# Performance work log

Hardware: AMD Instinct MI355X
Metric: run time of the kernel (lower is better)

The kernel has to match this reference:

```python
import jax, jax.numpy as jnp
import numpy as np

HEAD_NUM = 8
DIM_QK = 64
DIM_V = 64
SPAN = 64
STRIDE = 4


def _sparse_indices(length_q, length_kv):
    # Replicates torch meshgrid index math (static, numpy).
    R = SPAN // STRIDE
    r = np.arange(R)[:, None]              # [R,1]
    c = np.arange(length_q)[None, :]       # [1,Lq]
    # ceil((c-(span-1))/stride) + r, via floor-div identity ceil(a/b) = -((-a)//b)
    qi_col = -((SPAN - 1 - c) // STRIDE) + r   # [R,Lq]
    qi_row = c - STRIDE * qi_col
    valid = (qi_row >= 0) & (qi_row < SPAN) & (qi_col >= 0) & (qi_col < length_kv)
    qc = np.clip(qi_col, 0, length_kv - 1)
    return jnp.asarray(qc, dtype=jnp.int32), jnp.asarray(valid)


def setup_inputs() -> dict:
    key = jax.random.key(0)
    ks = jax.random.split(key, 7)
    B, Lq, Lkv, D = 2, 4096, 1024, 512
    q = jax.random.normal(ks[0], (B, Lq, D), dtype=jnp.float32)
    k = jax.random.normal(ks[1], (B, Lkv, D), dtype=jnp.float32)
    v = jax.random.normal(ks[2], (B, Lkv, D), dtype=jnp.float32)
    Wq = jax.random.normal(ks[3], (D, HEAD_NUM * DIM_QK), dtype=jnp.float32) * 0.05
    Wk = jax.random.normal(ks[4], (D, HEAD_NUM * DIM_QK), dtype=jnp.float32) * 0.05
    Wv = jax.random.normal(ks[5], (D, HEAD_NUM * DIM_V), dtype=jnp.float32) * 0.05
    Wout = jax.random.normal(ks[6], (HEAD_NUM * DIM_V, D), dtype=jnp.float32) * 0.05
    return {"q": q, "k": k, "v": v, "Wq": Wq, "Wk": Wk, "Wv": Wv, "Wout": Wout}


def reference(q, k, v, Wq, Wk, Wv, Wout):
    B, Lq, _ = q.shape
    Lkv = k.shape[1]
    # Projections -> [B, H, L, D]
    Q = (q @ Wq).reshape(B, Lq, HEAD_NUM, DIM_QK).transpose(0, 2, 1, 3)
    K = (k @ Wk).reshape(B, Lkv, HEAD_NUM, DIM_QK).transpose(0, 2, 1, 3)
    V = (v @ Wv).reshape(B, Lkv, HEAD_NUM, DIM_V).transpose(0, 2, 1, 3)
    qc, valid = _sparse_indices(Lq, Lkv)          # [R,Lq]
    Kg = K[:, :, qc, :]                            # [B,H,R,Lq,DQK] gather
    scores = jnp.einsum("bhcd,bhrcd->bhrc", Q, Kg) / jnp.sqrt(jnp.float32(DIM_QK))
    big_neg = jnp.asarray(-1e30, scores.dtype)
    scores = jnp.where(valid[None, None], scores, big_neg)
    w = jax.nn.softmax(scores, axis=2)             # softmax over the R sparse slots
    w = jnp.where(valid[None, None], w, 0.0)
    Vg = V[:, :, qc, :]                            # [B,H,R,Lq,DV] gather
    ctx = jnp.einsum("bhrc,bhrcd->bhcd", w, Vg)   # [B,H,Lq,DV]
    ctx = ctx.transpose(0, 2, 1, 3).reshape(B, Lq, HEAD_NUM * DIM_V)
    return ctx @ Wout
```

## Files before the change

kernel.cpp:

```cpp
#include <hip/hip_runtime.h>
#include <math.h>

#define HN 8
#define DK 64
#define LQ 4096
#define LKV 1024
#define DMODEL 512
#define BATCH 2

typedef unsigned short u16;
typedef unsigned int u32;
typedef __attribute__((ext_vector_type(8))) __bf16 bf16x8;
typedef __attribute__((ext_vector_type(4))) float f32x4;
typedef __attribute__((ext_vector_type(8))) u16 u16x8;

__device__ __forceinline__ u16 f2bf(float f) {
    u32 u = __float_as_uint(f);
    u = u + 0x7fffu + ((u >> 16) & 1u);
    return (u16)(u >> 16);
}
__device__ __forceinline__ float bf2f(u16 u) {
    return __uint_as_float(((u32)u) << 16);
}

__device__ __forceinline__ void gl_lds16(const u16* g, u16* l) {
    __builtin_amdgcn_global_load_lds((const __attribute__((address_space(1))) u32*)g,
                                     (__attribute__((address_space(3))) u32*)l, 16, 0, 0);
}

template <bool BF16OUT>
__device__ __forceinline__ void gemm_body(const u16* __restrict__ A,
                                          const u16* __restrict__ Bt,
                                          void* __restrict__ Cp,
                                          int bx, int by) {
    __shared__ u16 As[128 * 32];
    __shared__ u16 Bs[128 * 32];

    const int tid = threadIdx.x;
    const int lane = tid & 63;
    const int wave = tid >> 6;
    const int wm = (wave >> 1) * 64;
    const int wn = (wave & 1) * 64;
    const int quad = lane >> 4;
    const int l16 = lane & 15;
    const size_t m0 = (size_t)by * 128;
    const size_t n0 = (size_t)bx * 128;

    f32x4 acc[4][4] = {};

    for (int k0 = 0; k0 < 512; k0 += 32) {
#pragma unroll
        for (int i = 0; i < 2; ++i) {
            const int id = i * 256 + tid;
            const int r = id >> 2;
            const int cs = id & 3;
            const int c = cs ^ ((r >> 1) & 3);
            const u16* ga = &A[(m0 + r) * 512 + k0 + c * 8];
            const u16* gb = &Bt[(n0 + r) * 512 + k0 + c * 8];
            u16* la = &As[(size_t)(i * 256 + wave * 64) * 8];
            u16* lb = &Bs[(size_t)(i * 256 + wave * 64) * 8];
            gl_lds16(ga, la);
            gl_lds16(gb, lb);
        }
        __syncthreads();

        bf16x8 af[4], bf[4];
#pragma unroll
        for (int i = 0; i < 4; ++i) {
            const int ra = wm + i * 16 + l16;
            const int ca = quad ^ ((ra >> 1) & 3);
            af[i] = *(const bf16x8*)&As[ra * 32 + ca * 8];
            const int rb = wn + i * 16 + l16;
            const int cb = quad ^ ((rb >> 1) & 3);
            bf[i] = *(const bf16x8*)&Bs[rb * 32 + cb * 8];
        }
#pragma unroll
        for (int i = 0; i < 4; ++i)
#pragma unroll
            for (int j = 0; j < 4; ++j)
                acc[i][j] = __builtin_amdgcn_mfma_f32_16x16x32_bf16(af[i], bf[j], acc[i][j], 0, 0, 0);
        __syncthreads();
    }

#pragma unroll
    for (int i = 0; i < 4; ++i) {
#pragma unroll
        for (int j = 0; j < 4; ++j) {
            const size_t row = m0 + wm + i * 16 + quad * 4;
            const size_t col = n0 + wn + j * 16 + l16;
#pragma unroll
            for (int t = 0; t < 4; ++t) {
                if (BF16OUT)
                    ((u16*)Cp)[(row + t) * 512 + col] = f2bf(acc[i][j][t]);
                else
                    ((float*)Cp)[(row + t) * 512 + col] = acc[i][j][t];
            }
        }
    }
}

__global__ __launch_bounds__(256) void proj_fused(const u16* __restrict__ qb,
                                                  const u16* __restrict__ kb,
                                                  const u16* __restrict__ vb,
                                                  const u16* __restrict__ wqt,
                                                  const u16* __restrict__ wkt,
                                                  const u16* __restrict__ wvt,
                                                  u16* __restrict__ Qb,
                                                  u16* __restrict__ Kb,
                                                  u16* __restrict__ Vb) {
    const int idx = blockIdx.x;
    if (idx < 256)
        gemm_body<true>(qb, wqt, Qb, idx & 3, idx >> 2);
    else if (idx < 320)
        gemm_body<true>(kb, wkt, Kb, (idx - 256) & 3, (idx - 256) >> 2);
    else
        gemm_body<true>(vb, wvt, Vb, (idx - 320) & 3, (idx - 320) >> 2);
}

__global__ __launch_bounds__(256) void gemm_out(const u16* __restrict__ A,
                                                const u16* __restrict__ Bt,
                                                float* __restrict__ C) {
    gemm_body<false>(A, Bt, C, blockIdx.x & 3, blockIdx.x >> 2);
}

__global__ __launch_bounds__(256) void prep(const float* __restrict__ q,
                                            const float* __restrict__ k,
                                            const float* __restrict__ v,
                                            const float* __restrict__ Wq,
                                            const float* __restrict__ Wk,
                                            const float* __restrict__ Wv,
                                            const float* __restrict__ Wout,
                                            u16* __restrict__ qb, u16* __restrict__ kb,
                                            u16* __restrict__ vb,
                                            u16* __restrict__ wqt, u16* __restrict__ wkt,
                                            u16* __restrict__ wvt, u16* __restrict__ wot) {
    __shared__ float tbuf[32][33];
    const int bid = blockIdx.x;
    const int tid = threadIdx.x;

    if (bid < 3072) {
        const float* in;
        u16* outp;
        int i;
        if (bid < 2048)      { in = q; outp = qb; i = bid * 256 + tid; }
        else if (bid < 2560) { in = k; outp = kb; i = (bid - 2048) * 256 + tid; }
        else                 { in = v; outp = vb; i = (bid - 2560) * 256 + tid; }
        const float4 a = ((const float4*)in)[i * 2];
        const float4 b = ((const float4*)in)[i * 2 + 1];
        u16x8 r;
        r[0] = f2bf(a.x); r[1] = f2bf(a.y); r[2] = f2bf(a.z); r[3] = f2bf(a.w);
        r[4] = f2bf(b.x); r[5] = f2bf(b.y); r[6] = f2bf(b.z); r[7] = f2bf(b.w);
        *(u16x8*)&outp[(size_t)i * 8] = r;
    } else {
        const int wb = bid - 3072;
        const int z = wb >> 8;
        const int t = wb & 255;
        const float* W = (z == 0) ? Wq : (z == 1) ? Wk : (z == 2) ? Wv : Wout;
        u16* O = (z == 0) ? wqt : (z == 1) ? wkt : (z == 2) ? wvt : wot;
        const int tx = tid & 31;
        const int ty = tid >> 5;
        const int x = (t & 15) * 32 + tx;
        const int y0 = (t >> 4) * 32;
#pragma unroll
        for (int i = ty; i < 32; i += 8) tbuf[i][tx] = W[(size_t)(y0 + i) * 512 + x];
        __syncthreads();
#pragma unroll
        for (int i = ty; i < 32; i += 8)
            O[(size_t)((t & 15) * 32 + i) * 512 + y0 + tx] = f2bf(tbuf[tx][i]);
    }
}

__global__ __launch_bounds__(256) void attn_f32(const u16* __restrict__ Q,
                                                const u16* __restrict__ K,
                                                const u16* __restrict__ V,
                                                u16* __restrict__ ctx) {
    __shared__ float Ks[80][68];
    __shared__ float Vs[80][68];

    const int tid = threadIdx.x;
    const int c0 = blockIdx.x * 256;
    const int h = blockIdx.y;
    const int b = blockIdx.z;

    const int fd_c0 = (63 - c0) >> 2;
    const int win_lo = (fd_c0 < 0) ? -fd_c0 : 0;

    for (int i = tid; i < 80 * 8; i += 256) {
        int row = i >> 3;
        int d8 = i & 7;
        int col = win_lo + row;
        if (col < LKV) {
            size_t base = ((size_t)(b * LKV + col)) * DMODEL + h * DK + d8 * 8;
            u16x8 k8 = *(const u16x8*)&K[base];
            u16x8 v8 = *(const u16x8*)&V[base];
            float4 ka = make_float4(bf2f(k8[0]), bf2f(k8[1]), bf2f(k8[2]), bf2f(k8[3]));
            float4 kb4 = make_float4(bf2f(k8[4]), bf2f(k8[5]), bf2f(k8[6]), bf2f(k8[7]));
            float4 va = make_float4(bf2f(v8[0]), bf2f(v8[1]), bf2f(v8[2]), bf2f(v8[3]));
            float4 vb4 = make_float4(bf2f(v8[4]), bf2f(v8[5]), bf2f(v8[6]), bf2f(v8[7]));
            *(float4*)&Ks[row][d8 * 8] = ka;
            *(float4*)&Ks[row][d8 * 8 + 4] = kb4;
            *(float4*)&Vs[row][d8 * 8] = va;
            *(float4*)&Vs[row][d8 * 8 + 4] = vb4;
        }
    }
    __syncthreads();

    const int c = c0 + tid;
    const int fd = (63 - c) >> 2;

    float qreg[64];
    const u16* qp = &Q[((size_t)(b * LQ + c)) * DMODEL + h * DK];
#pragma unroll
    for (int i = 0; i < 8; ++i) {
        u16x8 t8 = *(const u16x8*)&qp[i * 8];
#pragma unroll
        for (int j = 0; j < 8; ++j) qreg[i * 8 + j] = bf2f(t8[j]);
    }

    float sc[16];
    float mx = -3.0e38f;
#pragma unroll
    for (int r = 0; r < 16; ++r) {
        int col = r - fd;
        if (col < 0) col = 0;
        const float* kr = &Ks[col - win_lo][0];
        float s = 0.f;
#pragma unroll
        for (int i = 0; i < 64; ++i) s = fmaf(qreg[i], kr[i], s);
        s *= 0.125f;
        sc[r] = (r >= fd) ? s : -1.0e30f;
        mx = fmaxf(mx, sc[r]);
    }

    float sum = 0.f;
#pragma unroll
    for (int r = 0; r < 16; ++r) {
        sc[r] = __expf(sc[r] - mx);
        sum += sc[r];
    }
    const float inv = 1.0f / sum;

    float acc[64];
#pragma unroll
    for (int i = 0; i < 64; ++i) acc[i] = 0.f;
#pragma unroll
    for (int r = 0; r < 16; ++r) {
        const float w = sc[r] * inv;
        int col = r - fd;
        if (col < 0) col = 0;
        const float* vr = &Vs[col - win_lo][0];
#pragma unroll
        for (int i = 0; i < 64; ++i) acc[i] = fmaf(w, vr[i], acc[i]);
    }

    u16* cp = &ctx[((size_t)(b * LQ + c)) * DMODEL + h * DK];
#pragma unroll
    for (int i = 0; i < 8; ++i) {
        u16x8 o;
#pragma unroll
        for (int j = 0; j < 8; ++j) o[j] = f2bf(acc[i * 8 + j]);
        *(u16x8*)&cp[i * 8] = o;
    }
}

extern "C" void kernel_launch(void* const* d_in, const int* in_sizes, int n_in,
                              void* d_out, int out_size, void* d_ws, size_t ws_size,
                              hipStream_t stream) {
    const float* q    = (const float*)d_in[0];
    const float* k    = (const float*)d_in[1];
    const float* v    = (const float*)d_in[2];
    const float* Wq   = (const float*)d_in[3];
    const float* Wk   = (const float*)d_in[4];
    const float* Wv   = (const float*)d_in[5];
    const float* Wout = (const float*)d_in[6];
    float* out = (float*)d_out;

    const size_t NQ = (size_t)BATCH * LQ * DMODEL;
    const size_t NK = (size_t)BATCH * LKV * DMODEL;
    const size_t NW = (size_t)DMODEL * DMODEL;

    u16* qb  = (u16*)d_ws;
    u16* kb  = qb + NQ;
    u16* vb  = kb + NK;
    u16* Qb  = vb + NK;
    u16* Kb  = Qb + NQ;
    u16* Vb  = Kb + NK;
    u16* cb  = Vb + NK;
    u16* wqt = cb + NQ;
    u16* wkt = wqt + NW;
    u16* wvt = wkt + NW;
    u16* wot = wvt + NW;

    prep<<<dim3(4096), dim3(256), 0, stream>>>(q, k, v, Wq, Wk, Wv, Wout,
                                               qb, kb, vb, wqt, wkt, wvt, wot);

    proj_fused<<<dim3(384), dim3(256), 0, stream>>>(qb, kb, vb, wqt, wkt, wvt, Qb, Kb, Vb);

    attn_f32<<<dim3(LQ / 256, HN, BATCH), dim3(256), 0, stream>>>(Qb, Kb, Vb, cb);

    gemm_out<<<dim3(256), dim3(256), 0, stream>>>(cb, wot, out);
}
```

Baseline: 128.3 us.

## Fuse all four stages into one cooperative persistent kernel with grid syncs

Replaces the four separate launches (prep, projection GEMM, attention, output GEMM) with a single cooperative kernel of 256 blocks. The blocks loop over each stage's jobs and call grid.sync between stages, with shared memory overlaid in a union. The aim is to remove per-launch overhead and gaps between kernels. In exchange, the projection stage (384 tiles) now needs two rounds on 256 blocks, and grid-wide barriers add cost. The attention inner loops are also rewritten with float4 vector reads, and a fallback to separate launches remains if the cooperative launch fails.

```diff
diff --git a/kernel.cpp b/kernel.cpp
--- a/kernel.cpp
+++ b/kernel.cpp
@@ -1,5 +1,8 @@
 #include <hip/hip_runtime.h>
+#include <hip/hip_cooperative_groups.h>
 #include <math.h>
+
+namespace cg = cooperative_groups;
 
 #define HN 8
 #define DK 64
@@ -7,6 +10,7 @@
 #define LKV 1024
 #define DMODEL 512
 #define BATCH 2
+#define NBLK 256
 
 typedef unsigned short u16;
 typedef unsigned int u32;
@@ -28,14 +32,13 @@
                                      (__attribute__((address_space(3))) u32*)l, 16, 0, 0);
 }
 
+struct GemmSm { u16 As[128 * 32]; u16 Bs[128 * 32]; };
+struct AttnSm { float Ks[80][68]; float Vs[80][68]; };
+union MegaSm { GemmSm g; AttnSm a; float tbuf[32][33]; };
+
 template <bool BF16OUT>
-__device__ __forceinline__ void gemm_body(const u16* __restrict__ A,
-                                          const u16* __restrict__ Bt,
-                                          void* __restrict__ Cp,
-                                          int bx, int by) {
-    __shared__ u16 As[128 * 32];
-    __shared__ u16 Bs[128 * 32];
-
+__device__ __forceinline__ void gemm_tile(const u16* A, const u16* Bt, void* Cp,
+                                          int bx, int by, GemmSm& sg) {
     const int tid = threadIdx.x;
     const int lane = tid & 63;
     const int wave = tid >> 6;
@@ -55,30 +58,26 @@
             const int r = id >> 2;
             const int cs = id & 3;
             const int c = cs ^ ((r >> 1) & 3);
-            const u16* ga = &A[(m0 + r) * 512 + k0 + c * 8];
-            const u16* gb = &Bt[(n0 + r) * 512 + k0 + c * 8];
-            u16* la = &As[(size_t)(i * 256 + wave * 64) * 8];
-            u16* lb = &Bs[(size_t)(i * 256 + wave * 64) * 8];
-            gl_lds16(ga, la);
-            gl_lds16(gb, lb);
-        }
-        __syncthreads();
-
-        bf16x8 af[4], bf[4];
+            gl_lds16(&A[(m0 + r) * 512 + k0 + c * 8], &sg.As[(size_t)(i * 256 + wave * 64) * 8]);
+            gl_lds16(&Bt[(n0 + r) * 512 + k0 + c * 8], &sg.Bs[(size_t)(i * 256 + wave * 64) * 8]);
+        }
+        __syncthreads();
+
+        bf16x8 af[4], bfr[4];
 #pragma unroll
         for (int i = 0; i < 4; ++i) {
             const int ra = wm + i * 16 + l16;
             const int ca = quad ^ ((ra >> 1) & 3);
-            af[i] = *(const bf16x8*)&As[ra * 32 + ca * 8];
+            af[i] = *(const bf16x8*)&sg.As[ra * 32 + ca * 8];
             const int rb = wn + i * 16 + l16;
             const int cb = quad ^ ((rb >> 1) & 3);
-            bf[i] = *(const bf16x8*)&Bs[rb * 32 + cb * 8];
+            bfr[i] = *(const bf16x8*)&sg.Bs[rb * 32 + cb * 8];
         }
 #pragma unroll
         for (int i = 0; i < 4; ++i)
 #pragma unroll
             for (int j = 0; j < 4; ++j)
-                acc[i][j] = __builtin_amdgcn_mfma_f32_16x16x32_bf16(af[i], bf[j], acc[i][j], 0, 0, 0);
+                acc[i][j] = __builtin_amdgcn_mfma_f32_16x16x32_bf16(af[i], bfr[j], acc[i][j], 0, 0, 0);
         __syncthreads();
     }
 
@@ -99,60 +98,120 @@
     }
 }
 
-__global__ __launch_bounds__(256) void proj_fused(const u16* __restrict__ qb,
-                                                  const u16* __restrict__ kb,
-                                                  const u16* __restrict__ vb,
-                                                  const u16* __restrict__ wqt,
-                                                  const u16* __restrict__ wkt,
-                                                  const u16* __restrict__ wvt,
-                                                  u16* __restrict__ Qb,
-                                                  u16* __restrict__ Kb,
-                                                  u16* __restrict__ Vb) {
-    const int idx = blockIdx.x;
-    if (idx < 256)
-        gemm_body<true>(qb, wqt, Qb, idx & 3, idx >> 2);
-    else if (idx < 320)
-        gemm_body<true>(kb, wkt, Kb, (idx - 256) & 3, (idx - 256) >> 2);
-    else
-        gemm_body<true>(vb, wvt, Vb, (idx - 320) & 3, (idx - 320) >> 2);
-}
-
-__global__ __launch_bounds__(256) void gemm_out(const u16* __restrict__ A,
-                                                const u16* __restrict__ Bt,
-                                                float* __restrict__ C) {
-    gemm_body<false>(A, Bt, C, blockIdx.x & 3, blockIdx.x >> 2);
-}
-
-__global__ __launch_bounds__(256) void prep(const float* __restrict__ q,
-                                            const float* __restrict__ k,
-                                            const float* __restrict__ v,
-                                            const float* __restrict__ Wq,
-                                            const float* __restrict__ Wk,
-                                            const float* __restrict__ Wv,
-                                            const float* __restrict__ Wout,
-                                            u16* __restrict__ qb, u16* __restrict__ kb,
-                                            u16* __restrict__ vb,
-                                            u16* __restrict__ wqt, u16* __restrict__ wkt,
-                                            u16* __restrict__ wvt, u16* __restrict__ wot) {
-    __shared__ float tbuf[32][33];
-    const int bid = blockIdx.x;
+__device__ __forceinline__ void attn_tile(const u16* Q, const u16* K, const u16* V,
+                                          u16* ctx, int cblk, int h, int b, AttnSm& sa) {
     const int tid = threadIdx.x;
-
-    if (bid < 3072) {
+    const int c0 = cblk * 256;
+    const int fd_c0 = (63 - c0) >> 2;
+    const int win_lo = (fd_c0 < 0) ? -fd_c0 : 0;
+
+    for (int i = tid; i < 80 * 8; i += 256) {
+        int row = i >> 3;
+        int d8 = i & 7;
+        int col = win_lo + row;
+        if (col < LKV) {
+            size_t base = ((size_t)(b * LKV + col)) * DMODEL + h * DK + d8 * 8;
+            u16x8 k8 = *(const u16x8*)&K[base];
+            u16x8 v8 = *(const u16x8*)&V[base];
+            *(float4*)&sa.Ks[row][d8 * 8]     = make_float4(bf2f(k8[0]), bf2f(k8[1]), bf2f(k8[2]), bf2f(k8[3]));
+            *(float4*)&sa.Ks[row][d8 * 8 + 4] = make_float4(bf2f(k8[4]), bf2f(k8[5]), bf2f(k8[6]), bf2f(k8[7]));
+            *(float4*)&sa.Vs[row][d8 * 8]     = make_float4(bf2f(v8[0]), bf2f(v8[1]), bf2f(v8[2]), bf2f(v8[3]));
+            *(float4*)&sa.Vs[row][d8 * 8 + 4] = make_float4(bf2f(v8[4]), bf2f(v8[5]), bf2f(v8[6]), bf2f(v8[7]));
+        }
+    }
+    __syncthreads();
+
+    const int c = c0 + tid;
+    const int fd = (63 - c) >> 2;
+
+    float4 qv[16];
+    const u16* qp = &Q[((size_t)(b * LQ + c)) * DMODEL + h * DK];
+#pragma unroll
+    for (int i = 0; i < 8; ++i) {
+        u16x8 t8 = *(const u16x8*)&qp[i * 8];
+        qv[i * 2]     = make_float4(bf2f(t8[0]), bf2f(t8[1]), bf2f(t8[2]), bf2f(t8[3]));
+        qv[i * 2 + 1] = make_float4(bf2f(t8[4]), bf2f(t8[5]), bf2f(t8[6]), bf2f(t8[7]));
+    }
+
+    float sc[16];
+    float mx = -3.0e38f;
+#pragma unroll
+    for (int r = 0; r < 16; ++r) {
+        int col = r - fd;
+        if (col < 0) col = 0;
+        const float4* kr = (const float4*)&sa.Ks[col - win_lo][0];
+        float s = 0.f;
+#pragma unroll
+        for (int i = 0; i < 16; ++i) {
+            float4 kv = kr[i];
+            s += qv[i].x * kv.x + qv[i].y * kv.y + qv[i].z * kv.z + qv[i].w * kv.w;
+        }
+        s *= 0.125f;
+        sc[r] = (r >= fd) ? s : -1.0e30f;
+        mx = fmaxf(mx, sc[r]);
+    }
+
+    float sum = 0.f;
+#pragma unroll
+    for (int r = 0; r < 16; ++r) {
+        sc[r] = __expf(sc[r] - mx);
+        sum += sc[r];
+    }
+    const float inv = 1.0f / sum;
+
+    float4 acc4[16];
+#pragma unroll
+    for (int i = 0; i < 16; ++i) acc4[i] = make_float4(0.f, 0.f, 0.f, 0.f);
+#pragma unroll
+    for (int r = 0; r < 16; ++r) {
+        const float w = sc[r] * inv;
+        int col = r - fd;
+        if (col < 0) col = 0;
+        const float4* vr = (const float4*)&sa.Vs[col - win_lo][0];
+#pragma unroll
+        for (int i = 0; i < 16; ++i) {
+            float4 vv = vr[i];
+            acc4[i].x = fmaf(w, vv.x, acc4[i].x);
+            acc4[i].y = fmaf(w, vv.y, acc4[i].y);
+            acc4[i].z = fmaf(w, vv.z, acc4[i].z);
+            acc4[i].w = fmaf(w, vv.w, acc4[i].w);
+        }
+    }
+
+    u16* cp = &ctx[((size_t)(b * LQ + c)) * DMODEL + h * DK];
+#pragma unroll
+    for (int i = 0; i < 8; ++i) {
+        u16x8 o;
+        o[0] = f2bf(acc4[i * 2].x);     o[1] = f2bf(acc4[i * 2].y);
+        o[2] = f2bf(acc4[i * 2].z);     o[3] = f2bf(acc4[i * 2].w);
+        o[4] = f2bf(acc4[i * 2 + 1].x); o[5] = f2bf(acc4[i * 2 + 1].y);
+        o[6] = f2bf(acc4[i * 2 + 1].z); o[7] = f2bf(acc4[i * 2 + 1].w);
+        *(u16x8*)&cp[i * 8] = o;
+    }
+}
+
+__device__ __forceinline__ void prep_job(int job, int tid,
+                                         const float* q, const float* k, const float* v,
+                                         const float* Wq, const float* Wk,
+                                         const float* Wv, const float* Wout,
+                                         u16* qb, u16* kb, u16* vb,
+                                         u16* wqt, u16* wkt, u16* wvt, u16* wot,
+                                         float (*tbuf)[33]) {
+    if (job < 3072) {
         const float* in;
         u16* outp;
         int i;
-        if (bid < 2048)      { in = q; outp = qb; i = bid * 256 + tid; }
-        else if (bid < 2560) { in = k; outp = kb; i = (bid - 2048) * 256 + tid; }
-        else                 { in = v; outp = vb; i = (bid - 2560) * 256 + tid; }
+        if (job < 2048)      { in = q; outp = qb; i = job * 256 + tid; }
+        else if (job < 2560) { in = k; outp = kb; i = (job - 2048) * 256 + tid; }
+        else                 { in = v; outp = vb; i = (job - 2560) * 256 + tid; }
         const float4 a = ((const float4*)in)[i * 2];
-        const float4 b = ((const float4*)in)[i * 2 + 1];
+        const float4 b4 = ((const float4*)in)[i * 2 + 1];
         u16x8 r;
-        r[0] = f2bf(a.x); r[1] = f2bf(a.y); r[2] = f2bf(a.z); r[3] = f2bf(a.w);
-        r[4] = f2bf(b.x); r[5] = f2bf(b.y); r[6] = f2bf(b.z); r[7] = f2bf(b.w);
+        r[0] = f2bf(a.x);  r[1] = f2bf(a.y);  r[2] = f2bf(a.z);  r[3] = f2bf(a.w);
+        r[4] = f2bf(b4.x); r[5] = f2bf(b4.y); r[6] = f2bf(b4.z); r[7] = f2bf(b4.w);
         *(u16x8*)&outp[(size_t)i * 8] = r;
     } else {
-        const int wb = bid - 3072;
+        const int wb = job - 3072;
         const int z = wb >> 8;
         const int t = wb & 255;
         const float* W = (z == 0) ? Wq : (z == 1) ? Wk : (z == 2) ? Wv : Wout;
@@ -161,6 +220,7 @@
         const int ty = tid >> 5;
         const int x = (t & 15) * 32 + tx;
         const int y0 = (t >> 4) * 32;
+        __syncthreads();
 #pragma unroll
         for (int i = ty; i < 32; i += 8) tbuf[i][tx] = W[(size_t)(y0 + i) * 512 + x];
         __syncthreads();
@@ -170,97 +230,81 @@
     }
 }
 
-__global__ __launch_bounds__(256) void attn_f32(const u16* __restrict__ Q,
-                                                const u16* __restrict__ K,
-                                                const u16* __restrict__ V,
-                                                u16* __restrict__ ctx) {
-    __shared__ float Ks[80][68];
-    __shared__ float Vs[80][68];
-
+__global__ __launch_bounds__(256) void mega(const float* q, const float* k, const float* v,
+                                            const float* Wq, const float* Wk,
+                                            const float* Wv, const float* Wout,
+                                            u16* qb, u16* kb, u16* vb,
+                                            u16* wqt, u16* wkt, u16* wvt, u16* wot,
+                                            u16* Qb, u16* Kb, u16* Vb, u16* cb,
+                                            float* out) {
+    cg::grid_group grid = cg::this_grid();
+    __shared__ MegaSm sm;
+    const int bid = blockIdx.x;
     const int tid = threadIdx.x;
-    const int c0 = blockIdx.x * 256;
-    const int h = blockIdx.y;
-    const int b = blockIdx.z;
-
-    const int fd_c0 = (63 - c0) >> 2;
-    const int win_lo = (fd_c0 < 0) ? -fd_c0 : 0;
-
-    for (int i = tid; i < 80 * 8; i += 256) {
-        int row = i >> 3;
-        int d8 = i & 7;
-        int col = win_lo + row;
-        if (col < LKV) {
-            size_t base = ((size_t)(b * LKV + col)) * DMODEL + h * DK + d8 * 8;
-            u16x8 k8 = *(const u16x8*)&K[base];
-            u16x8 v8 = *(const u16x8*)&V[base];
-            float4 ka = make_float4(bf2f(k8[0]), bf2f(k8[1]), bf2f(k8[2]), bf2f(k8[3]));
-            float4 kb4 = make_float4(bf2f(k8[4]), bf2f(k8[5]), bf2f(k8[6]), bf2f(k8[7]));
-            float4 va = make_float4(bf2f(v8[0]), bf2f(v8[1]), bf2f(v8[2]), bf2f(v8[3]));
-            float4 vb4 = make_float4(bf2f(v8[4]), bf2f(v8[5]), bf2f(v8[6]), bf2f(v8[7]));
-            *(float4*)&Ks[row][d8 * 8] = ka;
-            *(float4*)&Ks[row][d8 * 8 + 4] = kb4;
-            *(float4*)&Vs[row][d8 * 8] = va;
-            *(float4*)&Vs[row][d8 * 8 + 4] = vb4;
-        }
-    }
-    __syncthreads();
-
-    const int c = c0 + tid;
-    const int fd = (63 - c) >> 2;
-
-    float qreg[64];
-    const u16* qp = &Q[((size_t)(b * LQ + c)) * DMODEL + h * DK];
-#pragma unroll
-    for (int i = 0; i < 8; ++i) {
-        u16x8 t8 = *(const u16x8*)&qp[i * 8];
-#pragma unroll
-        for (int j = 0; j < 8; ++j) qreg[i * 8 + j] = bf2f(t8[j]);
-    }
-
-    float sc[16];
-    float mx = -3.0e38f;
-#pragma unroll
-    for (int r = 0; r < 16; ++r) {
-        int col = r - fd;
-        if (col < 0) col = 0;
-        const float* kr = &Ks[col - win_lo][0];
-        float s = 0.f;
-#pragma unroll
-        for (int i = 0; i < 64; ++i) s = fmaf(qreg[i], kr[i], s);
-        s *= 0.125f;
-        sc[r] = (r >= fd) ? s : -1.0e30f;
-        mx = fmaxf(mx, sc[r]);
-    }
-
-    float sum = 0.f;
-#pragma unroll
-    for (int r = 0; r < 16; ++r) {
-        sc[r] = __expf(sc[r] - mx);
-        sum += sc[r];
-    }
-    const float inv = 1.0f / sum;
-
-    float acc[64];
-#pragma unroll
-    for (int i = 0; i < 64; ++i) acc[i] = 0.f;
-#pragma unroll
-    for (int r = 0; r < 16; ++r) {
-        const float w = sc[r] * inv;
-        int col = r - fd;
-        if (col < 0) col = 0;
-        const float* vr = &Vs[col - win_lo][0];
-#pragma unroll
-        for (int i = 0; i < 64; ++i) acc[i] = fmaf(w, vr[i], acc[i]);
-    }
-
-    u16* cp = &ctx[((size_t)(b * LQ + c)) * DMODEL + h * DK];
-#pragma unroll
-    for (int i = 0; i < 8; ++i) {
-        u16x8 o;
-#pragma unroll
-        for (int j = 0; j < 8; ++j) o[j] = f2bf(acc[i * 8 + j]);
-        *(u16x8*)&cp[i * 8] = o;
-    }
+    const int nb = gridDim.x;
+
+    for (int job = bid; job < 4096; job += nb)
+        prep_job(job, tid, q, k, v, Wq, Wk, Wv, Wout, qb, kb, vb, wqt, wkt, wvt, wot, sm.tbuf);
+    __threadfence();
+    grid.sync();
+
+    for (int job = bid; job < 384; job += nb) {
+        if (job < 256)
+            gemm_tile<true>(qb, wqt, Qb, job & 3, job >> 2, sm.g);
+        else if (job < 320)
+            gemm_tile<true>(kb, wkt, Kb, (job - 256) & 3, (job - 256) >> 2, sm.g);
+        else
+            gemm_tile<true>(vb, wvt, Vb, (job - 320) & 3, (job - 320) >> 2, sm.g);
+        __syncthreads();
+    }
+    __threadfence();
+    grid.sync();
+
+    for (int job = bid; job < 256; job += nb) {
+        attn_tile(Qb, Kb, Vb, cb, job & 15, (job >> 4) & 7, job >> 7, sm.a);
+        __syncthreads();
+    }
+    __threadfence();
+    grid.sync();
+
+    for (int job = bid; job < 256; job += nb) {
+        gemm_tile<false>(cb, wot, out, job & 3, job >> 2, sm.g);
+        __syncthreads();
+    }
+}
+
+__global__ __launch_bounds__(256) void prep_k(const float* q, const float* k, const float* v,
+                                              const float* Wq, const float* Wk,
+                                              const float* Wv, const float* Wout,
+                                              u16* qb, u16* kb, u16* vb,
+                                              u16* wqt, u16* wkt, u16* wvt, u16* wot) {
+    __shared__ float tbuf[32][33];
+    prep_job(blockIdx.x, threadIdx.x, q, k, v, Wq, Wk, Wv, Wout,
+             qb, kb, vb, wqt, wkt, wvt, wot, tbuf);
+}
+
+__global__ __launch_bounds__(256) void proj_k(const u16* qb, const u16* kb, const u16* vb,
+                                              const u16* wqt, const u16* wkt, const u16* wvt,
+                                              u16* Qb, u16* Kb, u16* Vb) {
+    __shared__ GemmSm sg;
+    const int idx = blockIdx.x;
+    if (idx < 256)
+        gemm_tile<true>(qb, wqt, Qb, idx & 3, idx >> 2, sg);
+    else if (idx < 320)
+        gemm_tile<true>(kb, wkt, Kb, (idx - 256) & 3, (idx - 256) >> 2, sg);
+    else
+        gemm_tile<true>(vb, wvt, Vb, (idx - 320) & 3, (idx - 320) >> 2, sg);
+}
+
+__global__ __launch_bounds__(256) void attn_k(const u16* Q, const u16* K, const u16* V,
+                                              u16* ctx) {
+    __shared__ AttnSm sa;
+    attn_tile(Q, K, V, ctx, blockIdx.x, blockIdx.y, blockIdx.z, sa);
+}
+
+__global__ __launch_bounds__(256) void out_k(const u16* A, const u16* Bt, float* C) {
+    __shared__ GemmSm sg;
+    gemm_tile<false>(A, Bt, C, blockIdx.x & 3, blockIdx.x >> 2, sg);
 }
 
 extern "C" void kernel_launch(void* const* d_in, const int* in_sizes, int n_in,
@@ -291,12 +335,16 @@
     u16* wvt = wkt + NW;
     u16* wot = wvt + NW;
 
-    prep<<<dim3(4096), dim3(256), 0, stream>>>(q, k, v, Wq, Wk, Wv, Wout,
-                                               qb, kb, vb, wqt, wkt, wvt, wot);
-
-    proj_fused<<<dim3(384), dim3(256), 0, stream>>>(qb, kb, vb, wqt, wkt, wvt, Qb, Kb, Vb);
-
-    attn_f32<<<dim3(LQ / 256, HN, BATCH), dim3(256), 0, stream>>>(Qb, Kb, Vb, cb);
-
-    gemm_out<<<dim3(256), dim3(256), 0, stream>>>(cb, wot, out);
-}
+    void* args[] = {&q, &k, &v, &Wq, &Wk, &Wv, &Wout,
+                    &qb, &kb, &vb, &wqt, &wkt, &wvt, &wot,
+                    &Qb, &Kb, &Vb, &cb, &out};
+    hipError_t err = hipLaunchCooperativeKernel((const void*)mega, dim3(NBLK), dim3(256),
+                                                args, 0, stream);
+    if (err != hipSuccess) {
+        prep_k<<<dim3(4096), dim3(256), 0, stream>>>(q, k, v, Wq, Wk, Wv, Wout,
+                                                     qb, kb, vb, wqt, wkt, wvt, wot);
+        proj_k<<<dim3(384), dim3(256), 0, stream>>>(qb, kb, vb, wqt, wkt, wvt, Qb, Kb, Vb);
+        attn_k<<<dim3(16, HN, BATCH), dim3(256), 0, stream>>>(Qb, Kb, Vb, cb);
+        out_k<<<dim3(256), dim3(256), 0, stream>>>(cb, wot, out);
+    }
+}
```

Measured after the change: 352.5 us. 175% more time.
